# Optimization experiments

Hardware: AMD Instinct MI355X
Metric: run time of the kernel (lower is better)

The kernel has to match this reference:

```python
import jax, jax.numpy as jnp
import numpy as np

N, E, G = 20000, 320000, 256
F = 128
C = [256, 512, 1024]
NHID, NOUT = 1024, 768
EPS = 1e-5


def setup_inputs() -> dict:
    key = jax.random.key(0)
    keys = iter(jax.random.split(key, 64))
    def nrm(shape, s=0.02):
        return jax.random.normal(next(keys), shape, jnp.float32) * s
    inp = {}
    inp["x"] = jax.random.normal(next(keys), (N, F), jnp.float32)
    inp["edge_index"] = jax.random.randint(next(keys), (2, E), 0, N)
    inp["batch"] = jnp.sort(jax.random.randint(next(keys), (N,), 0, G))
    # stem GCNConv: F -> C[0]
    inp["w0"] = nrm((F, C[0])); inp["b0"] = jnp.zeros((C[0],), jnp.float32)
    # residual blocks
    for i in range(2):
        cin, cout = C[i], C[i + 1]
        mid = cin + (cout - cin) // 2
        p = f"blk{i}_"
        inp[p + "w1"] = nrm((cin, mid)); inp[p + "b1"] = jnp.zeros((mid,), jnp.float32)
        inp[p + "g1"] = jnp.ones((mid,), jnp.float32); inp[p + "be1"] = jnp.zeros((mid,), jnp.float32)
        inp[p + "w2"] = nrm((mid, cout)); inp[p + "b2"] = jnp.zeros((cout,), jnp.float32)
        inp[p + "g2"] = jnp.ones((cout,), jnp.float32); inp[p + "be2"] = jnp.zeros((cout,), jnp.float32)
        inp[p + "w3"] = nrm((cin, cout)); inp[p + "b3"] = jnp.zeros((cout,), jnp.float32)
    inp["mw1"] = nrm((C[-1], NHID)); inp["mb1"] = jnp.zeros((NHID,), jnp.float32)
    inp["mw2"] = nrm((NHID, NOUT)); inp["mb2"] = jnp.zeros((NOUT,), jnp.float32)
    return inp


def _gcn(x, w, b, src, dst, dinv):
    # PyG GCNConv: D^{-1/2}(A+I)D^{-1/2} X W + b, deg computed with self-loops
    xw = x @ w                                     # [N, Cout]
    msg = xw[src] * dinv[src, None]                # [E, Cout]
    agg = jax.ops.segment_sum(msg, dst, num_segments=x.shape[0])
    return agg * dinv[:, None] + xw * (dinv * dinv)[:, None] + b


def _bn(h, g, b):
    # BatchNorm1d in training mode: biased batch statistics over nodes
    m = h.mean(axis=0)
    v = h.var(axis=0)
    return g * (h - m) * jax.lax.rsqrt(v + EPS) + b


def reference(x, edge_index, batch, w0, b0,
              blk0_w1, blk0_b1, blk0_g1, blk0_be1, blk0_w2, blk0_b2, blk0_g2, blk0_be2, blk0_w3, blk0_b3,
              blk1_w1, blk1_b1, blk1_g1, blk1_be1, blk1_w2, blk1_b2, blk1_g2, blk1_be2, blk1_w3, blk1_b3,
              mw1, mb1, mw2, mb2):
    src, dst = edge_index[0], edge_index[1]
    deg = 1.0 + jax.ops.segment_sum(jnp.ones((src.shape[0],), x.dtype), dst, num_segments=x.shape[0])
    dinv = jax.lax.rsqrt(deg)                      # deg >= 1, no zero guard needed

    h = jax.nn.relu(_gcn(x, w0, b0, src, dst, dinv))
    blocks = [
        (blk0_w1, blk0_b1, blk0_g1, blk0_be1, blk0_w2, blk0_b2, blk0_g2, blk0_be2, blk0_w3, blk0_b3),
        (blk1_w1, blk1_b1, blk1_g1, blk1_be1, blk1_w2, blk1_b2, blk1_g2, blk1_be2, blk1_w3, blk1_b3),
    ]
    for (w1, b1, g1, be1, w2, b2, g2, be2, w3, b3) in blocks:
        t = jax.nn.relu(_bn(_gcn(h, w1, b1, src, dst, dinv), g1, be1))
        t = jax.nn.relu(_bn(_gcn(t, w2, b2, src, dst, dinv), g2, be2))
        h = jax.nn.relu(t) + _gcn(h, w3, b3, src, dst, dinv)

    # global mean pool over graphs
    s = jax.ops.segment_sum(h, batch, num_segments=G)
    cnt = jax.ops.segment_sum(jnp.ones((h.shape[0],), h.dtype), batch, num_segments=G)
    pooled = s / jnp.maximum(cnt, 1.0)[:, None]    # [G, C[-1]]

    out = jax.nn.relu(pooled @ mw1 + mb1) @ mw2 + mb2
    return out
```

## Files before the change

### kernel.cpp

```cpp
#include <hip/hip_runtime.h>
#include <cstdint>
#include <cstddef>

#define NN 20000
#define NE 320000
#define NG 256
#define NB 79

typedef unsigned short u16;
typedef __attribute__((ext_vector_type(8))) short bf16x8;
typedef __attribute__((ext_vector_type(4))) float f32x4;

__device__ inline float b2f(u16 h){
  union { unsigned u; float f; } v; v.u = ((unsigned)h) << 16; return v.f;
}
__device__ inline u16 f2b(float f){
  union { float f; unsigned u; } v; v.f = f;
  unsigned r = v.u + 0x7FFFu + ((v.u >> 16) & 1u);
  return (u16)(r >> 16);
}
__device__ inline void up8(const uint4& v, float* a){
  union { unsigned u; float f; } t;
  t.u = v.x << 16;         a[0] = t.f;
  t.u = v.x & 0xffff0000u; a[1] = t.f;
  t.u = v.y << 16;         a[2] = t.f;
  t.u = v.y & 0xffff0000u; a[3] = t.f;
  t.u = v.z << 16;         a[4] = t.f;
  t.u = v.z & 0xffff0000u; a[5] = t.f;
  t.u = v.w << 16;         a[6] = t.f;
  t.u = v.w & 0xffff0000u; a[7] = t.f;
}
__device__ inline unsigned pk2(float a, float b){
  return (unsigned)f2b(a) | (((unsigned)f2b(b)) << 16);
}
__device__ inline void bnrelu8(float* b, const float* sc, const float* sh){
  #pragma unroll
  for (int k = 0; k < 8; k++) b[k] = fmaxf(fmaf(b[k], sc[k], sh[k]), 0.f);
}

__device__ inline void gload_lds16(const void* g, void* l){
  __builtin_amdgcn_global_load_lds(
      (const __attribute__((address_space(1))) unsigned int*)g,
      (__attribute__((address_space(3))) unsigned int*)l, 16, 0, 0);
}


__global__ void k_zero(int* __restrict__ p, int n){
  int i = blockIdx.x*blockDim.x + threadIdx.x;
  if (i < n) p[i] = 0;
}

__global__ void k_deg(const int* __restrict__ ei, int* __restrict__ deg){
  int e = blockIdx.x*blockDim.x + threadIdx.x;
  if (e < NE) atomicAdd(&deg[ei[NE + e]], 1);
}

__global__ void k_scan1(const int* __restrict__ counts, int* __restrict__ bsum,
                        float* __restrict__ dinv){
  __shared__ int sm[256];
  int b = blockIdx.x, tid = threadIdx.x, idx = b*256 + tid;
  int v = (idx < NN) ? counts[idx] : 0;
  if (idx < NN) dinv[idx] = rsqrtf(1.0f + (float)v);
  sm[tid] = v;
  __syncthreads();
  for (int d = 128; d > 0; d >>= 1){
    if (tid < d) sm[tid] += sm[tid + d];
    __syncthreads();
  }
  if (tid == 0) bsum[b] = sm[0];
}
__global__ void k_scan2(int* __restrict__ bsum){
  if (threadIdx.x == 0){
    int c = 0;
    for (int i = 0; i < NB; i++){ int t = bsum[i]; bsum[i] = c; c += t; }
    bsum[NB] = c;
  }
}
__global__ void k_scan3(const int* __restrict__ counts, const int* __restrict__ bsum,
                        int* __restrict__ offs){
  __shared__ int sm[256];
  int b = blockIdx.x, tid = threadIdx.x, idx = b*256 + tid;
  int v = (idx < NN) ? counts[idx] : 0;
  sm[tid] = v;
  __syncthreads();
  for (int d = 1; d < 256; d <<= 1){
    int t = (tid >= d) ? sm[tid - d] : 0;
    __syncthreads();
    sm[tid] += t;
    __syncthreads();
  }
  if (idx < NN) offs[idx] = bsum[b] + sm[tid] - v;
  if (idx == NN - 1) offs[NN] = bsum[NB];
}

__global__ void k_fill(const int* __restrict__ ei, const int* __restrict__ offs,
                       int* __restrict__ cur, int* __restrict__ srcs){
  int e = blockIdx.x*blockDim.x + threadIdx.x;
  if (e < NE){
    int s = ei[e];
    int d = ei[NE + e];
    int p = atomicAdd(&cur[d], 1);
    srcs[offs[d] + p] = s;
  }
}

__global__ void k_bounds(const int* __restrict__ batch, int* __restrict__ start){
  int i = blockIdx.x*blockDim.x + threadIdx.x;
  if (i < NN){
    int b  = batch[i];
    int bp = (i == 0) ? -1 : batch[i-1];
    for (int g = bp + 1; g <= b; g++) start[g] = i;
    if (i == NN - 1){
      for (int g = b + 1; g <= NG; g++) start[g] = NN;
    }
  }
}

__global__ void k_cast(const float4* __restrict__ x, ushort4* __restrict__ xb, int total4){
  int t = blockIdx.x*blockDim.x + threadIdx.x;
  if (t >= total4) return;
  float4 v = x[t];
  ushort4 o; o.x = f2b(v.x); o.y = f2b(v.y); o.z = f2b(v.z); o.w = f2b(v.w);
  xb[t] = o;
}

struct WPArgs {
  const float* w[7];
  u16* wt[7];
  int K[7], N[7];
  int tstart[8];
};
__global__ __launch_bounds__(256) void k_wprep7(WPArgs a){
  __shared__ float sm[64][65];
  int bid = blockIdx.x;
  int wi = 0;
  while (wi < 6 && bid >= a.tstart[wi+1]) wi++;
  int tt = bid - a.tstart[wi];
  int K = a.K[wi], N = a.N[wi];
  int nk = K >> 6;
  int kb = (tt % nk) * 64, nb = (tt / nk) * 64;
  const float* w = a.w[wi];
  u16* wt = a.wt[wi];
  int tid = threadIdx.x;
  #pragma unroll
  for (int i = 0; i < 16; i++){
    int t = i*256 + tid;
    int r = t >> 6, c = t & 63;
    sm[r][c] = w[(size_t)(kb + r) * N + nb + c];
  }
  __syncthreads();
  #pragma unroll
  for (int i = 0; i < 16; i++){
    int t = i*256 + tid;
    int r = t >> 6, c = t & 63;
    wt[(size_t)(nb + r) * K + kb + c] = f2b(sm[c][r]);
  }
}

template<int C8, bool BN>
__global__ void k_agg_b(const uint4* __restrict__ in, uint4* __restrict__ out,
                        const float* __restrict__ dinv, const int* __restrict__ offs,
                        const int* __restrict__ srcs,
                        const float* __restrict__ sumv, const float* __restrict__ sqv,
                        const float* __restrict__ gam,  const float* __restrict__ bet){
  int t = blockIdx.x*blockDim.x + threadIdx.x;
  if (t >= NN * C8) return;
  int i = t / C8;
  int c = t - i * C8;
  float sc[8], sh[8];
  if (BN){
    #pragma unroll
    for (int k = 0; k < 8; k++){
      int ch = c*8 + k;
      float m  = sumv[ch] * (1.0f / NN);
      float vv = sqv[ch] * (1.0f / NN) - m * m;
      float rs = rsqrtf(vv + 1e-5f);
      sc[k] = gam[ch] * rs;
      sh[k] = bet[ch] - m * sc[k];
    }
  }
  float di = dinv[i];
  float a[8], acc[8];
  up8(in[t], a);
  if (BN) bnrelu8(a, sc, sh);
  #pragma unroll
  for (int k = 0; k < 8; k++) acc[k] = a[k] * di;

  int e = offs[i], e1 = offs[i + 1];
  for (; e + 4 <= e1; e += 4){
    int sA = srcs[e], sB = srcs[e+1], sC = srcs[e+2], sD = srcs[e+3];
    float dA = dinv[sA], dB = dinv[sB], dC = dinv[sC], dD = dinv[sD];
    uint4 yA = in[(size_t)sA * C8 + c];
    uint4 yB = in[(size_t)sB * C8 + c];
    uint4 yC = in[(size_t)sC * C8 + c];
    uint4 yD = in[(size_t)sD * C8 + c];
    float b[8];
    up8(yA, b);
    if (BN) bnrelu8(b, sc, sh);
    #pragma unroll
    for (int k = 0; k < 8; k++) acc[k] = fmaf(b[k], dA, acc[k]);
    up8(yB, b);
    if (BN) bnrelu8(b, sc, sh);
    #pragma unroll
    for (int k = 0; k < 8; k++) acc[k] = fmaf(b[k], dB, acc[k]);
    up8(yC, b);
    if (BN) bnrelu8(b, sc, sh);
    #pragma unroll
    for (int k = 0; k < 8; k++) acc[k] = fmaf(b[k], dC, acc[k]);
    up8(yD, b);
    if (BN) bnrelu8(b, sc, sh);
    #pragma unroll
    for (int k = 0; k < 8; k++) acc[k] = fmaf(b[k], dD, acc[k]);
  }
  for (; e < e1; e++){
    int s = srcs[e];
    float ds = dinv[s];
    float b[8];
    up8(in[(size_t)s * C8 + c], b);
    if (BN) bnrelu8(b, sc, sh);
    #pragma unroll
    for (int k = 0; k < 8; k++) acc[k] = fmaf(b[k], ds, acc[k]);
  }
  #pragma unroll
  for (int k = 0; k < 8; k++) acc[k] *= di;
  uint4 o;
  o.x = pk2(acc[0], acc[1]); o.y = pk2(acc[2], acc[3]);
  o.z = pk2(acc[4], acc[5]); o.w = pk2(acc[6], acc[7]);
  out[t] = o;
}

template<int MODE, bool STATS>
__global__ __launch_bounds__(256, 4) void k_mfma(const u16* __restrict__ A,
                                                 const u16* __restrict__ BT,
                                                 const float* __restrict__ bias,
                                                 u16* __restrict__ C,
                                                 float* __restrict__ p0,
                                                 float* __restrict__ p1,
                                                 const float* __restrict__ p2,
                                                 const float* __restrict__ p3,
                                                 int M, int K, int Nc){
  __shared__ u16 S[128*128];
  u16* As = S;
  u16* Bs = S + 128*64;
  const int tid = threadIdx.x;
  const int lane = tid & 63;
  const int quad = lane >> 4;
  const int l16 = lane & 15;
  const int wid = tid >> 6;
  const int wm = wid & 1, wn = wid >> 1;
  const int bm = blockIdx.x * 128, bn = blockIdx.y * 128;

  f32x4 acc[4][4];
  #pragma unroll
  for (int i = 0; i < 4; i++)
    #pragma unroll
    for (int j = 0; j < 4; j++)
      acc[i][j] = (f32x4){0.f, 0.f, 0.f, 0.f};

  const int srow = tid >> 3;
  const int scol8 = tid & 7;
  for (int k0 = 0; k0 < K; k0 += 64){
    #pragma unroll
    for (int i = 0; i < 4; i++){
      int row = i*32 + srow;
      int gc = (scol8 ^ (row & 7)) * 8;
      int lofs = row*64 + scol8*8;
      gload_lds16(A + (size_t)(bm + row) * K + k0 + gc, As + lofs);
      gload_lds16(BT + (size_t)(bn + row) * K + k0 + gc, Bs + lofs);
    }
    __syncthreads();
    #pragma unroll
    for (int kk = 0; kk < 2; kk++){
      const int col8 = kk*4 + quad;
      bf16x8 af[4], bfr[4];
      #pragma unroll
      for (int mi = 0; mi < 4; mi++){
        int row = wm*64 + mi*16 + l16;
        af[mi] = *(const bf16x8*)(As + row*64 + ((col8 ^ (row & 7)) * 8));
      }
      #pragma unroll
      for (int ni = 0; ni < 4; ni++){
        int row = wn*64 + ni*16 + l16;
        bfr[ni] = *(const bf16x8*)(Bs + row*64 + ((col8 ^ (row & 7)) * 8));
      }
      #pragma unroll
      for (int mi = 0; mi < 4; mi++)
        #pragma unroll
        for (int ni = 0; ni < 4; ni++)
          acc[mi][ni] = __builtin_amdgcn_mfma_f32_16x16x32_bf16(af[mi], bfr[ni], acc[mi][ni], 0, 0, 0);
    }
    __syncthreads();
  }
  #pragma unroll
  for (int ni = 0; ni < 4; ni++){
    int colL = wn*64 + ni*16 + l16;
    float bb = bias[bn + colL];
    float s = 0.f, s2 = 0.f;
    #pragma unroll
    for (int mi = 0; mi < 4; mi++){
      int rbase = wm*64 + mi*16 + quad*4;
      #pragma unroll
      for (int r = 0; r < 4; r++){
        int rowL = rbase + r;
        float v = acc[mi][ni][r] + bb;
        if (STATS && (bm + rowL) < M){ s += v; s2 += v * v; }
        if (MODE == 1) v = fmaxf(v, 0.f);
        S[rowL*128 + colL] = f2b(v);
      }
    }
    if (STATS){
      s  += __shfl_xor(s, 16, 64);  s  += __shfl_xor(s, 32, 64);
      s2 += __shfl_xor(s2, 16, 64); s2 += __shfl_xor(s2, 32, 64);
      if (quad == 0){
        atomicAdd(&p0[bn + colL], s);
        atomicAdd(&p1[bn + colL], s2);
      }
    }
  }
  __syncthreads();
  #pragma unroll
  for (int it = 0; it < 8; it++){
    int idx = it*256 + tid;
    int rl = idx >> 4, cq = idx & 15;
    int row = bm + rl;
    if (row < M){
      int col0 = bn + cq*8;
      uint4 w = *(const uint4*)(S + rl*128 + cq*8);
      u16* cp = C + (size_t)row * Nc + col0;
      if (MODE == 3){
        float o[8], ov[8];
        up8(w, o);
        uint4 old = *(const uint4*)cp;
        up8(old, ov);
        #pragma unroll
        for (int k = 0; k < 8; k++){
          int ch = col0 + k;
          float m  = p0[ch] * (1.0f / NN);
          float vv = p1[ch] * (1.0f / NN) - m * m;
          float rs = rsqrtf(vv + 1e-5f);
          float sc = p2[ch] * rs;
          float sh = p3[ch] - m * sc;
          o[k] += fmaxf(fmaf(ov[k], sc, sh), 0.f);
        }
        uint4 ou;
        ou.x = pk2(o[0], o[1]); ou.y = pk2(o[2], o[3]);
        ou.z = pk2(o[4], o[5]); ou.w = pk2(o[6], o[7]);
        *(uint4*)cp = ou;
      } else {
        *(uint4*)cp = w;
      }
    }
  }
}

template<bool RELUA>
__global__ __launch_bounds__(256) void k_gemm_sk(const float* __restrict__ A,
                                                 const float* __restrict__ B,
                                                 const float* __restrict__ bias,
                                                 float* __restrict__ C,
                                                 int M, int K, int Nc){
  __shared__ float As[16][68];
  __shared__ float Bs[16][64];
  const int tid = threadIdx.x;
  const int tx = tid & 15, ty = tid >> 4;
  const int bm = blockIdx.x * 64, bn = blockIdx.y * 64;
  const int kchunk = K / gridDim.z;
  const int ks = blockIdx.z * kchunk, ke = ks + kchunk;
  const int arow = tid >> 2, akq = (tid & 3) << 2;
  const int brow = tid >> 4, bcol = (tid & 15) << 2;
  float acc[4][4] = {{0.f}};
  const bool aval = (bm + arow) < M;
  const float* Aptr = A + (size_t)(bm + arow) * K + akq;
  const float* Bptr = B + (size_t)brow * Nc + bn + bcol;
  for (int k0 = ks; k0 < ke; k0 += 16){
    float4 av = make_float4(0.f, 0.f, 0.f, 0.f);
    if (aval) av = *(const float4*)(Aptr + k0);
    if (RELUA){
      av.x = fmaxf(av.x, 0.f); av.y = fmaxf(av.y, 0.f);
      av.z = fmaxf(av.z, 0.f); av.w = fmaxf(av.w, 0.f);
    }
    float4 bv = *(const float4*)(Bptr + (size_t)k0 * Nc);
    As[akq + 0][arow] = av.x;
    As[akq + 1][arow] = av.y;
    As[akq + 2][arow] = av.z;
    As[akq + 3][arow] = av.w;
    *(float4*)&Bs[brow][bcol] = bv;
    __syncthreads();
    #pragma unroll
    for (int kk = 0; kk < 16; kk++){
      const float4 a = *(const float4*)(&As[kk][ty << 2]);
      const float4 b = *(const float4*)(&Bs[kk][tx << 2]);
      const float ar[4] = {a.x, a.y, a.z, a.w};
      const float br[4] = {b.x, b.y, b.z, b.w};
      #pragma unroll
      for (int i = 0; i < 4; i++)
        #pragma unroll
        for (int j = 0; j < 4; j++)
          acc[i][j] = fmaf(ar[i], br[j], acc[i][j]);
    }
    __syncthreads();
  }
  const int col = bn + (tx << 2);
  float4 bb = make_float4(0.f, 0.f, 0.f, 0.f);
  if (blockIdx.z == 0) bb = *(const float4*)(bias + col);
  #pragma unroll
  for (int i = 0; i < 4; i++){
    int row = bm + (ty << 2) + i;
    if (row < M){
      float* cp = C + (size_t)row * Nc + col;
      atomicAdd(cp + 0, acc[i][0] + bb.x);
      atomicAdd(cp + 1, acc[i][1] + bb.y);
      atomicAdd(cp + 2, acc[i][2] + bb.z);
      atomicAdd(cp + 3, acc[i][3] + bb.w);
    }
  }
}

__global__ __launch_bounds__(256) void k_pool_b(const u16* __restrict__ h,
                                                const int* __restrict__ start,
                                                float* __restrict__ pooled){
  __shared__ float sm[128*8];
  int g = blockIdx.x;
  int half = threadIdx.x >> 7;
  int cb = threadIdx.x & 127;
  int c = cb << 3;
  int r0 = start[g], r1 = start[g + 1];
  float acc[8] = {0.f,0.f,0.f,0.f,0.f,0.f,0.f,0.f};
  for (int r = r0 + half; r < r1; r += 2){
    float b[8];
    up8(*(const uint4*)(h + (size_t)r * 1024 + c), b);
    #pragma unroll
    for (int k = 0; k < 8; k++) acc[k] += b[k];
  }
  if (half){
    #pragma unroll
    for (int k = 0; k < 8; k++) sm[cb*8 + k] = acc[k];
  }
  __syncthreads();
  if (!half){
    float inv = (r1 > r0) ? (1.0f / (float)(r1 - r0)) : 0.0f;
    float o[8];
    #pragma unroll
    for (int k = 0; k < 8; k++) o[k] = (acc[k] + sm[cb*8 + k]) * inv;
    float4* dst = (float4*)(pooled + (size_t)g * 1024 + c);
    dst[0] = make_float4(o[0], o[1], o[2], o[3]);
    dst[1] = make_float4(o[4], o[5], o[6], o[7]);
  }
}


extern "C" void kernel_launch(void* const* d_in, const int* in_sizes, int n_in,
                              void* d_out, int out_size, void* d_ws, size_t ws_size,
                              hipStream_t stream) {
  const float* x    = (const float*)d_in[0];
  const int*   ei   = (const int*)d_in[1];
  const int*   bat  = (const int*)d_in[2];
  const float* w0   = (const float*)d_in[3];
  const float* b0   = (const float*)d_in[4];
  const float* a_w1 = (const float*)d_in[5],  *a_b1  = (const float*)d_in[6];
  const float* a_g1 = (const float*)d_in[7],  *a_be1 = (const float*)d_in[8];
  const float* a_w2 = (const float*)d_in[9],  *a_b2  = (const float*)d_in[10];
  const float* a_g2 = (const float*)d_in[11], *a_be2 = (const float*)d_in[12];
  const float* a_w3 = (const float*)d_in[13], *a_b3  = (const float*)d_in[14];
  const float* c_w1 = (const float*)d_in[15], *c_b1  = (const float*)d_in[16];
  const float* c_g1 = (const float*)d_in[17], *c_be1 = (const float*)d_in[18];
  const float* c_w2 = (const float*)d_in[19], *c_b2  = (const float*)d_in[20];
  const float* c_g2 = (const float*)d_in[21], *c_be2 = (const float*)d_in[22];
  const float* c_w3 = (const float*)d_in[23], *c_b3  = (const float*)d_in[24];
  const float* mw1  = (const float*)d_in[25], *mb1   = (const float*)d_in[26];
  const float* mw2  = (const float*)d_in[27], *mb2   = (const float*)d_in[28];
  float* out = (float*)d_out;

  char* pp = (char*)d_ws;
  auto alloc = [&](size_t b)->char*{ char* r = pp; pp += (b + 255) & ~(size_t)255; return r; };

  const size_t CH = (size_t)NN * 2;
  char* R = alloc(2304 * CH);
  float* dinv = (float*)alloc((size_t)NN * 4);
  int* icomb  = (int*)alloc((size_t)2 * NN * 4);
  int* deg    = icomb;
  int* cur    = icomb + NN;
  int* offs   = (int*)alloc((size_t)(NN + 1) * 4);
  int* bsum   = (int*)alloc((size_t)(NB + 1) * 4);
  int* srcs   = (int*)alloc((size_t)NE * 4);
  int* startg = (int*)alloc((size_t)(NG + 1) * 4);
  float* SB   = (float*)alloc(5376 * 4);
  float* sA1 = SB;
  float* sA2 = SB + 768;
  float* sC1 = SB + 1792;
  float* sC2 = SB + 3328;
  u16* WT  = (u16*)alloc(2162688 * 2);
  u16* wt0  = WT;
  u16* wtA1 = WT + 32768;
  u16* wtA2 = WT + 131072;
  u16* wtA3 = WT + 327680;
  u16* wtC1 = WT + 458752;
  u16* wtC2 = WT + 851968;
  u16* wtC3 = WT + 1638400;
  float* P  = (float*)WT;
  float* Hh = P + (size_t)NG * 1024;

  auto slot = [&](int s)->u16*{ return (u16*)(R + (size_t)s * CH); };
  u16* xb  = slot(512);
  u16* ax  = slot(0);
  u16* h0  = slot(128);
  u16* ah0 = slot(1664);
  u16* t1  = slot(1920);
  u16* at  = slot(1280);
  u16* h1  = slot(768);
  u16* ah1 = slot(1792);
  u16* u1  = slot(0);
  u16* au  = slot(1024);
  u16* h2  = slot(0);

  auto cdiv = [](int a, int b){ return (a + b - 1) / b; };

  k_zero<<<cdiv(2*NN,256),256,0,stream>>>(icomb, 2*NN);
  k_zero<<<cdiv(5376,256),256,0,stream>>>((int*)SB, 5376);
  k_deg <<<cdiv(NE,256),256,0,stream>>>(ei, deg);
  k_scan1<<<NB,256,0,stream>>>(deg, bsum, dinv);
  k_scan2<<<1,64,0,stream>>>(bsum);
  k_scan3<<<NB,256,0,stream>>>(deg, bsum, offs);
  k_fill<<<cdiv(NE,256),256,0,stream>>>(ei, offs, cur, srcs);
  k_bounds<<<cdiv(NN,256),256,0,stream>>>(bat, startg);
  k_cast<<<cdiv(NN*32,256),256,0,stream>>>((const float4*)x, (ushort4*)xb, NN*32);

  {
    WPArgs wa;
    const float* ws[7] = {w0, a_w1, a_w2, a_w3, c_w1, c_w2, c_w3};
    u16* wts[7] = {wt0, wtA1, wtA2, wtA3, wtC1, wtC2, wtC3};
    int Ks[7] = {128, 256, 384, 256, 512, 768, 512};
    int Ns[7] = {256, 384, 512, 512, 768, 1024, 1024};
    int acc = 0;
    for (int i = 0; i < 7; i++){
      wa.w[i] = ws[i]; wa.wt[i] = wts[i]; wa.K[i] = Ks[i]; wa.N[i] = Ns[i];
      wa.tstart[i] = acc;
      acc += (Ks[i]/64) * (Ns[i]/64);
    }
    wa.tstart[7] = acc;
    k_wprep7<<<acc,256,0,stream>>>(wa);
  }

  auto agg = [&](const u16* in, u16* o, int C, const float* st,
                 const float* g, const float* be){
    int C8 = C / 8;
    int gb = cdiv(NN * C8, 256);
    if (!st){
      switch (C8){
        case 16: k_agg_b<16,false><<<gb,256,0,stream>>>((const uint4*)in,(uint4*)o,dinv,offs,srcs,nullptr,nullptr,nullptr,nullptr); break;
        case 32: k_agg_b<32,false><<<gb,256,0,stream>>>((const uint4*)in,(uint4*)o,dinv,offs,srcs,nullptr,nullptr,nullptr,nullptr); break;
        case 64: k_agg_b<64,false><<<gb,256,0,stream>>>((const uint4*)in,(uint4*)o,dinv,offs,srcs,nullptr,nullptr,nullptr,nullptr); break;
        default: break;
      }
    } else {
      switch (C8){
        case 48: k_agg_b<48,true><<<gb,256,0,stream>>>((const uint4*)in,(uint4*)o,dinv,offs,srcs,st,st+C,g,be); break;
        case 96: k_agg_b<96,true><<<gb,256,0,stream>>>((const uint4*)in,(uint4*)o,dinv,offs,srcs,st,st+C,g,be); break;
        default: break;
      }
    }
  };
  auto gemm_m = [&](const u16* A, const u16* BT_, const float* bi, u16* Cc,
                    int K, int Nc, int mode, float* st, int sC,
                    const float* g2, const float* b2){
    dim3 g(cdiv(NN,128), Nc/128);
    if (mode == 0)
      k_mfma<0,true><<<g,256,0,stream>>>(A, BT_, bi, Cc, st, st + sC, nullptr, nullptr, NN, K, Nc);
    else if (mode == 1)
      k_mfma<1,false><<<g,256,0,stream>>>(A, BT_, bi, Cc, nullptr, nullptr, nullptr, nullptr, NN, K, Nc);
    else
      k_mfma<3,false><<<g,256,0,stream>>>(A, BT_, bi, Cc, st, st + sC, g2, b2, NN, K, Nc);
  };

  agg(xb, ax, 128, nullptr, nullptr, nullptr);
  gemm_m(ax, wt0, b0, h0, 128, 256, 1, nullptr, 0, nullptr, nullptr);
  agg(h0, ah0, 256, nullptr, nullptr, nullptr);
  gemm_m(ah0, wtA1, a_b1, t1, 256, 384, 0, sA1, 384, nullptr, nullptr);
  agg(t1, at, 384, sA1, a_g1, a_be1);
  gemm_m(at, wtA2, a_b2, h1, 384, 512, 0, sA2, 512, nullptr, nullptr);
  gemm_m(ah0, wtA3, a_b3, h1, 256, 512, 3, sA2, 512, a_g2, a_be2);
  agg(h1, ah1, 512, nullptr, nullptr, nullptr);
  gemm_m(ah1, wtC1, c_b1, u1, 512, 768, 0, sC1, 768, nullptr, nullptr);
  agg(u1, au, 768, sC1, c_g1, c_be1);
  gemm_m(au, wtC2, c_b2, h2, 768, 1024, 0, sC2, 1024, nullptr, nullptr);
  gemm_m(ah1, wtC3, c_b3, h2, 512, 1024, 3, sC2, 1024, c_g2, c_be2);
  k_pool_b<<<NG,256,0,stream>>>(h2, startg, P);
  {
    k_zero<<<cdiv(NG*1024,256),256,0,stream>>>((int*)Hh, NG*1024);
    k_zero<<<cdiv(NG*768,256),256,0,stream>>>((int*)out, NG*768);
    dim3 g1(cdiv(NG,64), 1024/64, 8);
    k_gemm_sk<false><<<g1,256,0,stream>>>(P, mw1, mb1, Hh, NG, 1024, 1024);
    dim3 g2(cdiv(NG,64), 768/64, 8);
    k_gemm_sk<true><<<g2,256,0,stream>>>(Hh, mw2, mb2, out, NG, 1024, 768);
  }
}
```

Baseline: 670.4 us.

## Partition aggregation columns into XCD-mapped groups and use nontemporal stores

The sparse aggregation kernel now splits feature columns into 8 groups selected by the low bits of the block index. Under round-robin block dispatch across chiplets, each group's gathered slice of the input can stay resident in one L2 instead of thrashing across all of them. Output writes use nontemporal stores to avoid polluting cache. The cost is shorter contiguous reads per node row and reliance on the block-to-XCD dispatch pattern.

```diff
diff --git a/kernel.cpp b/kernel.cpp
--- a/kernel.cpp
+++ b/kernel.cpp
@@ -10,6 +10,7 @@
 typedef unsigned short u16;
 typedef __attribute__((ext_vector_type(8))) short bf16x8;
 typedef __attribute__((ext_vector_type(4))) float f32x4;
+typedef __attribute__((ext_vector_type(4))) unsigned int u32x4;
 
 __device__ inline float b2f(u16 h){
   union { unsigned u; float f; } v; v.u = ((unsigned)h) << 16; return v.f;
@@ -157,16 +158,18 @@
   }
 }
 
-template<int C8, bool BN>
-__global__ void k_agg_b(const uint4* __restrict__ in, uint4* __restrict__ out,
+template<int C8, int C8G, bool BN>
+__global__ __launch_bounds__(256) void k_agg_b(const uint4* __restrict__ in, uint4* __restrict__ out,
                         const float* __restrict__ dinv, const int* __restrict__ offs,
                         const int* __restrict__ srcs,
                         const float* __restrict__ sumv, const float* __restrict__ sqv,
                         const float* __restrict__ gam,  const float* __restrict__ bet){
-  int t = blockIdx.x*blockDim.x + threadIdx.x;
-  if (t >= NN * C8) return;
-  int i = t / C8;
-  int c = t - i * C8;
+  int bid = blockIdx.x;
+  int g = bid & 7;
+  int t = (bid >> 3)*256 + threadIdx.x;
+  if (t >= NN * C8G) return;
+  int i = t / C8G;
+  int c = g * C8G + (t - i * C8G);
   float sc[8], sh[8];
   if (BN){
     #pragma unroll
@@ -181,7 +184,7 @@
   }
   float di = dinv[i];
   float a[8], acc[8];
-  up8(in[t], a);
+  up8(in[(size_t)i * C8 + c], a);
   if (BN) bnrelu8(a, sc, sh);
   #pragma unroll
   for (int k = 0; k < 8; k++) acc[k] = a[k] * di;
@@ -223,10 +226,10 @@
   }
   #pragma unroll
   for (int k = 0; k < 8; k++) acc[k] *= di;
-  uint4 o;
+  u32x4 o;
   o.x = pk2(acc[0], acc[1]); o.y = pk2(acc[2], acc[3]);
   o.z = pk2(acc[4], acc[5]); o.w = pk2(acc[6], acc[7]);
-  out[t] = o;
+  __builtin_nontemporal_store(o, (u32x4*)&out[(size_t)i * C8 + c]);
 }
 
 template<int MODE, bool STATS>
@@ -544,18 +547,19 @@
   auto agg = [&](const u16* in, u16* o, int C, const float* st,
                  const float* g, const float* be){
     int C8 = C / 8;
-    int gb = cdiv(NN * C8, 256);
+    int C8G = C8 / 8;
+    int gb = 8 * cdiv(NN * C8G, 256);
     if (!st){
       switch (C8){
-        case 16: k_agg_b<16,false><<<gb,256,0,stream>>>((const uint4*)in,(uint4*)o,dinv,offs,srcs,nullptr,nullptr,nullptr,nullptr); break;
-        case 32: k_agg_b<32,false><<<gb,256,0,stream>>>((const uint4*)in,(uint4*)o,dinv,offs,srcs,nullptr,nullptr,nullptr,nullptr); break;
-        case 64: k_agg_b<64,false><<<gb,256,0,stream>>>((const uint4*)in,(uint4*)o,dinv,offs,srcs,nullptr,nullptr,nullptr,nullptr); break;
+        case 16: k_agg_b<16,2,false><<<gb,256,0,stream>>>((const uint4*)in,(uint4*)o,dinv,offs,srcs,nullptr,nullptr,nullptr,nullptr); break;
+        case 32: k_agg_b<32,4,false><<<gb,256,0,stream>>>((const uint4*)in,(uint4*)o,dinv,offs,srcs,nullptr,nullptr,nullptr,nullptr); break;
+        case 64: k_agg_b<64,8,false><<<gb,256,0,stream>>>((const uint4*)in,(uint4*)o,dinv,offs,srcs,nullptr,nullptr,nullptr,nullptr); break;
         default: break;
       }
     } else {
       switch (C8){
-        case 48: k_agg_b<48,true><<<gb,256,0,stream>>>((const uint4*)in,(uint4*)o,dinv,offs,srcs,st,st+C,g,be); break;
-        case 96: k_agg_b<96,true><<<gb,256,0,stream>>>((const uint4*)in,(uint4*)o,dinv,offs,srcs,st,st+C,g,be); break;
+        case 48: k_agg_b<48,6,true><<<gb,256,0,stream>>>((const uint4*)in,(uint4*)o,dinv,offs,srcs,st,st+C,g,be); break;
+        case 96: k_agg_b<96,12,true><<<gb,256,0,stream>>>((const uint4*)in,(uint4*)o,dinv,offs,srcs,st,st+C,g,be); break;
         default: break;
       }
     }
```

Result: slower. 687.6 us (+2.6%).

## Pre-scale features by dinv and split wide aggregations into channel groups

Applied to the files above, without the earlier changes.

Source features are multiplied by dinv[src] before aggregation: in the input cast, in GEMM epilogues, and in new in-place BN+ReLU+scale kernels. The gather loop then only sums neighbour rows and skips the per-edge dinv loads and BN math. For the wide layers (384/512/768 channels), the aggregation is split into 8 channel groups on the block index, so concurrently running blocks touch a narrower slice of the feature matrix, which is meant to improve cache reuse. The cost is an extra read-modify-write pass for the BN layers and pre-scaled values rounded to bf16 before summation.

```diff
diff --git a/kernel.cpp b/kernel.cpp
--- a/kernel.cpp
+++ b/kernel.cpp
@@ -116,11 +116,14 @@
   }
 }
 
-__global__ void k_cast(const float4* __restrict__ x, ushort4* __restrict__ xb, int total4){
+__global__ void k_cast(const float4* __restrict__ x, ushort4* __restrict__ xb,
+                       const float* __restrict__ dinv, int total4){
   int t = blockIdx.x*blockDim.x + threadIdx.x;
   if (t >= total4) return;
+  float di = dinv[t >> 5];
   float4 v = x[t];
-  ushort4 o; o.x = f2b(v.x); o.y = f2b(v.y); o.z = f2b(v.z); o.w = f2b(v.w);
+  ushort4 o; o.x = f2b(v.x * di); o.y = f2b(v.y * di);
+  o.z = f2b(v.z * di); o.w = f2b(v.w * di);
   xb[t] = o;
 }
 
@@ -157,10 +160,9 @@
   }
 }
 
-template<int C8, bool BN>
-__global__ void k_agg_b(const uint4* __restrict__ in, uint4* __restrict__ out,
-                        const float* __restrict__ dinv, const int* __restrict__ offs,
-                        const int* __restrict__ srcs,
+template<int C8>
+__global__ __launch_bounds__(256) void k_bnscale(uint4* __restrict__ buf,
+                        const float* __restrict__ dinv,
                         const float* __restrict__ sumv, const float* __restrict__ sqv,
                         const float* __restrict__ gam,  const float* __restrict__ bet){
   int t = blockIdx.x*blockDim.x + threadIdx.x;
@@ -168,68 +170,77 @@
   int i = t / C8;
   int c = t - i * C8;
   float sc[8], sh[8];
-  if (BN){
-    #pragma unroll
-    for (int k = 0; k < 8; k++){
-      int ch = c*8 + k;
-      float m  = sumv[ch] * (1.0f / NN);
-      float vv = sqv[ch] * (1.0f / NN) - m * m;
-      float rs = rsqrtf(vv + 1e-5f);
-      sc[k] = gam[ch] * rs;
-      sh[k] = bet[ch] - m * sc[k];
-    }
+  #pragma unroll
+  for (int k = 0; k < 8; k++){
+    int ch = c*8 + k;
+    float m  = sumv[ch] * (1.0f / NN);
+    float vv = sqv[ch] * (1.0f / NN) - m * m;
+    float rs = rsqrtf(vv + 1e-5f);
+    sc[k] = gam[ch] * rs;
+    sh[k] = bet[ch] - m * sc[k];
   }
   float di = dinv[i];
-  float a[8], acc[8];
-  up8(in[t], a);
-  if (BN) bnrelu8(a, sc, sh);
-  #pragma unroll
-  for (int k = 0; k < 8; k++) acc[k] = a[k] * di;
-
+  float a[8];
+  up8(buf[t], a);
+  #pragma unroll
+  for (int k = 0; k < 8; k++) a[k] = fmaxf(fmaf(a[k], sc[k], sh[k]), 0.f) * di;
+  uint4 o;
+  o.x = pk2(a[0], a[1]); o.y = pk2(a[2], a[3]);
+  o.z = pk2(a[4], a[5]); o.w = pk2(a[6], a[7]);
+  buf[t] = o;
+}
+
+template<int C8, int C8G>
+__global__ __launch_bounds__(256) void k_agg_b(const uint4* __restrict__ in, uint4* __restrict__ out,
+                        const float* __restrict__ dinv, const int* __restrict__ offs,
+                        const int* __restrict__ srcs){
+  constexpr bool PART = (C8G != C8);
+  int bid = blockIdx.x;
+  int g = PART ? (bid & 7) : 0;
+  int t = PART ? ((bid >> 3)*256 + threadIdx.x) : (bid*256 + threadIdx.x);
+  if (t >= NN * C8G) return;
+  int i = t / C8G;
+  int c = g * C8G + (t - i * C8G);
+  float acc[8];
+  up8(in[(size_t)i * C8 + c], acc);
   int e = offs[i], e1 = offs[i + 1];
   for (; e + 4 <= e1; e += 4){
     int sA = srcs[e], sB = srcs[e+1], sC = srcs[e+2], sD = srcs[e+3];
-    float dA = dinv[sA], dB = dinv[sB], dC = dinv[sC], dD = dinv[sD];
     uint4 yA = in[(size_t)sA * C8 + c];
     uint4 yB = in[(size_t)sB * C8 + c];
     uint4 yC = in[(size_t)sC * C8 + c];
     uint4 yD = in[(size_t)sD * C8 + c];
     float b[8];
     up8(yA, b);
-    if (BN) bnrelu8(b, sc, sh);
-    #pragma unroll
-    for (int k = 0; k < 8; k++) acc[k] = fmaf(b[k], dA, acc[k]);
+    #pragma unroll
+    for (int k = 0; k < 8; k++) acc[k] += b[k];
     up8(yB, b);
-    if (BN) bnrelu8(b, sc, sh);
-    #pragma unroll
-    for (int k = 0; k < 8; k++) acc[k] = fmaf(b[k], dB, acc[k]);
+    #pragma unroll
+    for (int k = 0; k < 8; k++) acc[k] += b[k];
     up8(yC, b);
-    if (BN) bnrelu8(b, sc, sh);
-    #pragma unroll
-    for (int k = 0; k < 8; k++) acc[k] = fmaf(b[k], dC, acc[k]);
+    #pragma unroll
+    for (int k = 0; k < 8; k++) acc[k] += b[k];
     up8(yD, b);
-    if (BN) bnrelu8(b, sc, sh);
-    #pragma unroll
-    for (int k = 0; k < 8; k++) acc[k] = fmaf(b[k], dD, acc[k]);
+    #pragma unroll
+    for (int k = 0; k < 8; k++) acc[k] += b[k];
   }
   for (; e < e1; e++){
     int s = srcs[e];
-    float ds = dinv[s];
     float b[8];
     up8(in[(size_t)s * C8 + c], b);
-    if (BN) bnrelu8(b, sc, sh);
-    #pragma unroll
-    for (int k = 0; k < 8; k++) acc[k] = fmaf(b[k], ds, acc[k]);
-  }
+    #pragma unroll
+    for (int k = 0; k < 8; k++) acc[k] += b[k];
+  }
+  float di = dinv[i];
   #pragma unroll
   for (int k = 0; k < 8; k++) acc[k] *= di;
   uint4 o;
   o.x = pk2(acc[0], acc[1]); o.y = pk2(acc[2], acc[3]);
   o.z = pk2(acc[4], acc[5]); o.w = pk2(acc[6], acc[7]);
-  out[t] = o;
-}
-
-template<int MODE, bool STATS>
+  out[(size_t)i * C8 + c] = o;
+}
+
+template<int MODE, bool STATS, bool SCALE>
 __global__ __launch_bounds__(256, 4) void k_mfma(const u16* __restrict__ A,
                                                  const u16* __restrict__ BT,
                                                  const float* __restrict__ bias,
@@ -238,6 +249,7 @@
                                                  float* __restrict__ p1,
                                                  const float* __restrict__ p2,
                                                  const float* __restrict__ p3,
+                                                 const float* __restrict__ dv,
                                                  int M, int K, int Nc){
   __shared__ u16 S[128*128];
   u16* As = S;
@@ -328,6 +340,7 @@
       uint4 w = *(const uint4*)(S + rl*128 + cq*8);
       u16* cp = C + (size_t)row * Nc + col0;
       if (MODE == 3){
+        float di = SCALE ? dv[row] : 1.f;
         float o[8], ov[8];
         up8(w, o);
         uint4 old = *(const uint4*)cp;
@@ -341,7 +354,18 @@
           float sc = p2[ch] * rs;
           float sh = p3[ch] - m * sc;
           o[k] += fmaxf(fmaf(ov[k], sc, sh), 0.f);
+          if (SCALE) o[k] *= di;
         }
+        uint4 ou;
+        ou.x = pk2(o[0], o[1]); ou.y = pk2(o[2], o[3]);
+        ou.z = pk2(o[4], o[5]); ou.w = pk2(o[6], o[7]);
+        *(uint4*)cp = ou;
+      } else if (SCALE){
+        float di = dv[row];
+        float o[8];
+        up8(w, o);
+        #pragma unroll
+        for (int k = 0; k < 8; k++) o[k] *= di;
         uint4 ou;
         ou.x = pk2(o[0], o[1]); ou.y = pk2(o[2], o[3]);
         ou.z = pk2(o[4], o[5]); ou.w = pk2(o[6], o[7]);
@@ -523,7 +547,7 @@
   k_scan3<<<NB,256,0,stream>>>(deg, bsum, offs);
   k_fill<<<cdiv(NE,256),256,0,stream>>>(ei, offs, cur, srcs);
   k_bounds<<<cdiv(NN,256),256,0,stream>>>(bat, startg);
-  k_cast<<<cdiv(NN*32,256),256,0,stream>>>((const float4*)x, (ushort4*)xb, NN*32);
+  k_cast<<<cdiv(NN*32,256),256,0,stream>>>((const float4*)x, (ushort4*)xb, dinv, NN*32);
 
   {
     WPArgs wa;
@@ -541,49 +565,45 @@
     k_wprep7<<<acc,256,0,stream>>>(wa);
   }
 
-  auto agg = [&](const u16* in, u16* o, int C, const float* st,
-                 const float* g, const float* be){
+  auto agg = [&](const u16* in, u16* o, int C){
     int C8 = C / 8;
-    int gb = cdiv(NN * C8, 256);
-    if (!st){
-      switch (C8){
-        case 16: k_agg_b<16,false><<<gb,256,0,stream>>>((const uint4*)in,(uint4*)o,dinv,offs,srcs,nullptr,nullptr,nullptr,nullptr); break;
-        case 32: k_agg_b<32,false><<<gb,256,0,stream>>>((const uint4*)in,(uint4*)o,dinv,offs,srcs,nullptr,nullptr,nullptr,nullptr); break;
-        case 64: k_agg_b<64,false><<<gb,256,0,stream>>>((const uint4*)in,(uint4*)o,dinv,offs,srcs,nullptr,nullptr,nullptr,nullptr); break;
-        default: break;
-      }
-    } else {
-      switch (C8){
-        case 48: k_agg_b<48,true><<<gb,256,0,stream>>>((const uint4*)in,(uint4*)o,dinv,offs,srcs,st,st+C,g,be); break;
-        case 96: k_agg_b<96,true><<<gb,256,0,stream>>>((const uint4*)in,(uint4*)o,dinv,offs,srcs,st,st+C,g,be); break;
-        default: break;
-      }
+    switch (C8){
+      case 16: k_agg_b<16,16><<<cdiv(NN*16,256),256,0,stream>>>((const uint4*)in,(uint4*)o,dinv,offs,srcs); break;
+      case 32: k_agg_b<32,32><<<cdiv(NN*32,256),256,0,stream>>>((const uint4*)in,(uint4*)o,dinv,offs,srcs); break;
+      case 48: k_agg_b<48, 6><<<8*cdiv(NN*6,256),256,0,stream>>>((const uint4*)in,(uint4*)o,dinv,offs,srcs); break;
+      case 64: k_agg_b<64, 8><<<8*cdiv(NN*8,256),256,0,stream>>>((const uint4*)in,(uint4*)o,dinv,offs,srcs); break;
+      case 96: k_agg_b<96,12><<<8*cdiv(NN*12,256),256,0,stream>>>((const uint4*)in,(uint4*)o,dinv,offs,srcs); break;
+      default: break;
     }
   };
   auto gemm_m = [&](const u16* A, const u16* BT_, const float* bi, u16* Cc,
                     int K, int Nc, int mode, float* st, int sC,
-                    const float* g2, const float* b2){
+                    const float* g2, const float* b2, bool scale3){
     dim3 g(cdiv(NN,128), Nc/128);
     if (mode == 0)
-      k_mfma<0,true><<<g,256,0,stream>>>(A, BT_, bi, Cc, st, st + sC, nullptr, nullptr, NN, K, Nc);
+      k_mfma<0,true,false><<<g,256,0,stream>>>(A, BT_, bi, Cc, st, st + sC, nullptr, nullptr, dinv, NN, K, Nc);
     else if (mode == 1)
-      k_mfma<1,false><<<g,256,0,stream>>>(A, BT_, bi, Cc, nullptr, nullptr, nullptr, nullptr, NN, K, Nc);
+      k_mfma<1,false,true><<<g,256,0,stream>>>(A, BT_, bi, Cc, nullptr, nullptr, nullptr, nullptr, dinv, NN, K, Nc);
+    else if (scale3)
+      k_mfma<3,false,true><<<g,256,0,stream>>>(A, BT_, bi, Cc, st, st + sC, g2, b2, dinv, NN, K, Nc);
     else
-      k_mfma<3,false><<<g,256,0,stream>>>(A, BT_, bi, Cc, st, st + sC, g2, b2, NN, K, Nc);
+      k_mfma<3,false,false><<<g,256,0,stream>>>(A, BT_, bi, Cc, st, st + sC, g2, b2, dinv, NN, K, Nc);
   };
 
-  agg(xb, ax, 128, nullptr, nullptr, nullptr);
-  gemm_m(ax, wt0, b0, h0, 128, 256, 1, nullptr, 0, nullptr, nullptr);
-  agg(h0, ah0, 256, nullptr, nullptr, nullptr);
-  gemm_m(ah0, wtA1, a_b1, t1, 256, 384, 0, sA1, 384, nullptr, nullptr);
-  agg(t1, at, 384, sA1, a_g1, a_be1);
-  gemm_m(at, wtA2, a_b2, h1, 384, 512, 0, sA2, 512, nullptr, nullptr);
-  gemm_m(ah0, wtA3, a_b3, h1, 256, 512, 3, sA2, 512, a_g2, a_be2);
-  agg(h1, ah1, 512, nullptr, nullptr, nullptr);
-  gemm_m(ah1, wtC1, c_b1, u1, 512, 768, 0, sC1, 768, nullptr, nullptr);
-  agg(u1, au, 768, sC1, c_g1, c_be1);
-  gemm_m(au, wtC2, c_b2, h2, 768, 1024, 0, sC2, 1024, nullptr, nullptr);
-  gemm_m(ah1, wtC3, c_b3, h2, 512, 1024, 3, sC2, 1024, c_g2, c_be2);
+  agg(xb, ax, 128);
+  gemm_m(ax, wt0, b0, h0, 128, 256, 1, nullptr, 0, nullptr, nullptr, false);
+  agg(h0, ah0, 256);
+  gemm_m(ah0, wtA1, a_b1, t1, 256, 384, 0, sA1, 384, nullptr, nullptr, false);
+  k_bnscale<48><<<cdiv(NN*48,256),256,0,stream>>>((uint4*)t1, dinv, sA1, sA1+384, a_g1, a_be1);
+  agg(t1, at, 384);
+  gemm_m(at, wtA2, a_b2, h1, 384, 512, 0, sA2, 512, nullptr, nullptr, false);
+  gemm_m(ah0, wtA3, a_b3, h1, 256, 512, 3, sA2, 512, a_g2, a_be2, true);
+  agg(h1, ah1, 512);
+  gemm_m(ah1, wtC1, c_b1, u1, 512, 768, 0, sC1, 768, nullptr, nullptr, false);
+  k_bnscale<96><<<cdiv(NN*96,256),256,0,stream>>>((uint4*)u1, dinv, sC1, sC1+768, c_g1, c_be1);
+  agg(u1, au, 768);
+  gemm_m(au, wtC2, c_b2, h2, 768, 1024, 0, sC2, 1024, nullptr, nullptr, false);
+  gemm_m(ah1, wtC3, c_b3, h2, 512, 1024, 3, sC2, 1024, c_g2, c_be2, false);
   k_pool_b<<<NG,256,0,stream>>>(h2, startg, P);
   {
     k_zero<<<cdiv(NG*1024,256),256,0,stream>>>((int*)Hh, NG*1024);
```

New measurement: 659.4 us. No clear change (-1.6%).
